# Optimization experiments

Hardware: AMD Instinct MI355X
Metric: run time of the kernel (lower is better)

## Reference

```python
import jax, jax.numpy as jnp
import numpy as np

B, N = 8, 2048
D_MODEL, D_QK, NHEAD, N_K, D_FF = 256, 128, 8, 16, 1024
LN_EPS = 1e-5


def _layer_norm(x, g, b):
    m = jnp.mean(x, axis=-1, keepdims=True)
    v = jnp.var(x, axis=-1, keepdims=True)
    return (x - m) * jax.lax.rsqrt(v + LN_EPS) * g + b


def _l2_normalize(x):
    # F.normalize(dim=-1): x / max(||x||_2, 1e-12)
    n = jnp.sqrt(jnp.sum(x * x, axis=-1, keepdims=True))
    return x / jnp.maximum(n, 1e-12)


def setup_inputs() -> dict:
    key = jax.random.key(0)
    ks = jax.random.split(key, 12)
    s = 0.02
    return {
        "x": jax.random.normal(ks[0], (B, N, D_MODEL), dtype=jnp.float32),
        # linear_q / linear_k (d_model -> d_model_qk)
        "Wq": jax.random.normal(ks[1], (D_MODEL, D_QK), dtype=jnp.float32) * s,
        "bq": jnp.zeros((D_QK,), jnp.float32),
        "Wk": jax.random.normal(ks[2], (D_MODEL, D_QK), dtype=jnp.float32) * s,
        "bk": jnp.zeros((D_QK,), jnp.float32),
        # NoLinearQKMHA: value + output projections (d_model -> d_model)
        "Wv": jax.random.normal(ks[3], (D_MODEL, D_MODEL), dtype=jnp.float32) * s,
        "bv": jnp.zeros((D_MODEL,), jnp.float32),
        "Wo": jax.random.normal(ks[4], (D_MODEL, D_MODEL), dtype=jnp.float32) * s,
        "bo": jnp.zeros((D_MODEL,), jnp.float32),
        # norm1 (applied to gathered values)
        "g1": jnp.ones((D_MODEL,), jnp.float32),
        "b1": jnp.zeros((D_MODEL,), jnp.float32),
        # ffn: LayerNorm -> Linear -> GELU -> Linear
        "gf": jnp.ones((D_MODEL,), jnp.float32),
        "bf": jnp.zeros((D_MODEL,), jnp.float32),
        "W1": jax.random.normal(ks[5], (D_MODEL, D_FF), dtype=jnp.float32) * s,
        "b1f": jnp.zeros((D_FF,), jnp.float32),
        "W2": jax.random.normal(ks[6], (D_FF, D_MODEL), dtype=jnp.float32) * s,
        "b2f": jnp.zeros((D_MODEL,), jnp.float32),
        # residual_weight (init 0 in torch; nonzero here for a meaningful baseline)
        "rw": jnp.full((1,), 0.5, jnp.float32),
    }


def reference(x, Wq, bq, Wk, bk, Wv, bv, Wo, bo, g1, b1, gf, bf, W1, b1f, W2, b2f, rw):
    # --- project + normalize queries/keys ---
    qn = _l2_normalize(x @ Wq + bq)   # [B,N,Dqk]
    kn = _l2_normalize(x @ Wk + bk)   # [B,N,Dqk]

    # --- KNN: k smallest Euclidean distances from each query to keys ---
    d2 = (jnp.sum(qn * qn, -1)[:, :, None]
          + jnp.sum(kn * kn, -1)[:, None, :]
          - 2.0 * jnp.einsum('bqd,bkd->bqk', qn, kn))   # [B,N,N]
    _, idx = jax.lax.top_k(-d2, N_K)                     # [B,N,n_k]

    # --- gather neighbors ---
    gather = jax.vmap(lambda arr, ind: arr[ind])
    x_v = gather(x, idx)    # [B,N,n_k,D_MODEL]
    x_k = gather(kn, idx)   # [B,N,n_k,Dqk]

    # --- windowed MHA (NoLinearQK: q,k used directly; v projected) ---
    xnorm = _layer_norm(x_v, g1, b1)
    v = xnorm @ Wv + bv                                  # [B,N,n_k,D_MODEL]
    dh, dv = D_QK // NHEAD, D_MODEL // NHEAD
    qh = qn.reshape(B, N, NHEAD, dh)
    kh = x_k.reshape(B, N, N_K, NHEAD, dh)
    vh = v.reshape(B, N, N_K, NHEAD, dv)
    logits = jnp.einsum('bnhd,bnkhd->bnhk', qh, kh) / np.float32(np.sqrt(dh))
    attn = jax.nn.softmax(logits, axis=-1)
    o = jnp.einsum('bnhk,bnkhe->bnhe', attn, vh).reshape(B, N, D_MODEL)
    o = o @ Wo + bo

    # --- residuals (eval: dropout = identity) ---
    x = x + o * rw
    h = _layer_norm(x, gf, bf) @ W1 + b1f
    h = jax.nn.gelu(h, approximate=False) @ W2 + b2f
    x = x + h * rw
    return x
```

## Files before the change

kernel.cpp:

```cpp
#include <hip/hip_runtime.h>
#include <math.h>

#define BATCH 8
#define SEQ   2048
#define DM    256
#define DQK   128
#define NHEADS 8
#define NK    16
#define DFF   1024

typedef __attribute__((ext_vector_type(8))) short short8;
typedef __attribute__((ext_vector_type(8))) _Float16 half8;
typedef __attribute__((ext_vector_type(4))) float floatx4;
typedef unsigned long long ull;

__device__ __forceinline__ unsigned short f2bf(float f) {
    unsigned int u = __float_as_uint(f);
    u += 0x7fffu + ((u >> 16) & 1u);
    return (unsigned short)(u >> 16);
}

__device__ __forceinline__ float gelu_fast(float h) {
    float y = 0.7978845608028654f * (h + 0.044715f * h * h * h);
    float e = __expf(2.f * y);
    float t = 1.f - 2.f / (e + 1.f);
    return 0.5f * h * (1.f + t);
}

__device__ __forceinline__ ull mkkey(float f, int gidx) {
    unsigned int u = __float_as_uint(f);
    u ^= (unsigned int)((int)u >> 31) | 0x80000000u;
    return ((ull)u << 32) | (unsigned int)(2047 - gidx);
}

__device__ __forceinline__ ull shfl_xor_u64(ull v, int m) {
    unsigned int lo = (unsigned int)v, hi = (unsigned int)(v >> 32);
    lo = __shfl_xor(lo, m);
    hi = __shfl_xor(hi, m);
    return ((ull)hi << 32) | lo;
}

__global__ __launch_bounds__(256) void conv_kernel(
    const float* __restrict__ W1, const float* __restrict__ W2,
    const float* __restrict__ Wv, const float* __restrict__ Wo,
    unsigned short* __restrict__ W1f, unsigned short* __restrict__ W2f,
    unsigned short* __restrict__ Wvf, unsigned short* __restrict__ Wof)
{
    int g = blockIdx.x * 256 + threadIdx.x;
    const float* W; unsigned short* O; int e, stride;
    if (g < 32768)      { W = W1; O = W1f; e = g;         stride = DFF; }
    else if (g < 65536) { W = W2; O = W2f; e = g - 32768; stride = DM;  }
    else if (g < 73728) { W = Wv; O = Wvf; e = g - 65536; stride = DM;  }
    else                { W = Wo; O = Wof; e = g - 73728; stride = DM;  }
    int lane = e & 63;
    int kk, nt;
    if (g < 32768)      { kk = (e >> 6) & 7;  nt = e >> 9;  }
    else if (g < 65536) { kk = (e >> 6) & 31; nt = e >> 11; }
    else                { kk = (e >> 6) & 7;  nt = e >> 9;  }
    int n = nt * 16 + (lane & 15);
    int k0 = kk * 32 + (lane >> 4) * 8;
    unsigned int pk[4];
    #pragma unroll
    for (int jj = 0; jj < 4; ++jj) {
        unsigned short lo = f2bf(W[(size_t)(k0 + 2 * jj) * stride + n]);
        unsigned short hi = f2bf(W[(size_t)(k0 + 2 * jj + 1) * stride + n]);
        pk[jj] = (unsigned int)lo | ((unsigned int)hi << 16);
    }
    *(uint4*)(O + (size_t)e * 8) = make_uint4(pk[0], pk[1], pk[2], pk[3]);
}

__global__ __launch_bounds__(256) void proj_qk_kernel(
    const float* __restrict__ x,
    const float* __restrict__ Wq, const float* __restrict__ bq,
    const float* __restrict__ Wk, const float* __restrict__ bk,
    float* __restrict__ qn, float* __restrict__ kn,
    unsigned short* __restrict__ knTh, unsigned short* __restrict__ knTl,
    float* __restrict__ knsq)
{
    __shared__ __align__(16) float xs[8 * 256];
    __shared__ __align__(16) float ks[8 * 128];
    __shared__ float nred[8][2], kred[8][2], k2red[8][2];

    const int tid = threadIdx.x;
    const int b = blockIdx.x & 7;
    const int chunk = blockIdx.x >> 3;
    const size_t t0 = (size_t)b * SEQ + (size_t)chunk * 8;

    for (int i = tid; i < 8 * 256; i += 256) xs[i] = x[t0 * DM + i];
    __syncthreads();

    {
        const int col = tid & 127, half = tid >> 7;
        float qa[4] = {0.f, 0.f, 0.f, 0.f}, ka[4] = {0.f, 0.f, 0.f, 0.f};
        for (int d = 0; d < 256; ++d) {
            float wq = Wq[d * DQK + col];
            float wk = Wk[d * DQK + col];
            #pragma unroll
            for (int t = 0; t < 4; ++t) {
                float xv = xs[(half * 4 + t) * 256 + d];
                qa[t] = fmaf(xv, wq, qa[t]);
                ka[t] = fmaf(xv, wk, ka[t]);
            }
        }
        #pragma unroll
        for (int t = 0; t < 4; ++t) { qa[t] += bq[col]; ka[t] += bk[col]; }

        const int sub = (tid >> 6) & 1;
        #pragma unroll
        for (int t = 0; t < 4; ++t) {
            float sq = qa[t] * qa[t], sk = ka[t] * ka[t];
            #pragma unroll
            for (int m = 1; m < 64; m <<= 1) { sq += __shfl_xor(sq, m); sk += __shfl_xor(sk, m); }
            if ((tid & 63) == 0) { nred[half * 4 + t][sub] = sq; kred[half * 4 + t][sub] = sk; }
        }
        __syncthreads();
        float kvv[4];
        #pragma unroll
        for (int t = 0; t < 4; ++t) {
            int tok = half * 4 + t;
            float nq = sqrtf(nred[tok][0] + nred[tok][1]);
            float nk = sqrtf(kred[tok][0] + kred[tok][1]);
            float qv = qa[t] / fmaxf(nq, 1e-12f);
            float kv = ka[t] / fmaxf(nk, 1e-12f);
            qn[(t0 + tok) * DQK + col] = qv;
            kn[(t0 + tok) * DQK + col] = kv;
            ks[tok * 128 + col] = kv;
            kvv[t] = kv;
        }
        #pragma unroll
        for (int t = 0; t < 4; ++t) {
            float s2 = kvv[t] * kvv[t];
            #pragma unroll
            for (int m = 1; m < 64; m <<= 1) s2 += __shfl_xor(s2, m);
            if ((tid & 63) == 0) k2red[half * 4 + t][sub] = s2;
        }
        __syncthreads();
        if (tid < 8) knsq[t0 + tid] = k2red[tid][0] + k2red[tid][1];
    }

    {
        const int e   = tid & 127;
        const int sel = tid >> 7;
        const int key = e & 7;
        const int kq  = e >> 3;
        const int kk  = kq >> 2, qd = kq & 3;
        const int nt  = chunk >> 1;
        const int n   = ((chunk & 1) << 3) + key;
        const float* src = &ks[key * 128 + kk * 32 + qd * 8];
        unsigned int pk[4];
        #pragma unroll
        for (int jj = 0; jj < 4; ++jj) {
            float v0 = src[2 * jj], v1 = src[2 * jj + 1];
            _Float16 h0 = (_Float16)v0, h1 = (_Float16)v1;
            unsigned short u0, u1;
            if (sel == 0) {
                u0 = __builtin_bit_cast(unsigned short, h0);
                u1 = __builtin_bit_cast(unsigned short, h1);
            } else {
                _Float16 l0 = (_Float16)((v0 - (float)h0) * 4096.f);
                _Float16 l1 = (_Float16)((v1 - (float)h1) * 4096.f);
                u0 = __builtin_bit_cast(unsigned short, l0);
                u1 = __builtin_bit_cast(unsigned short, l1);
            }
            pk[jj] = (unsigned int)u0 | ((unsigned int)u1 << 16);
        }
        unsigned short* dst = (sel ? knTl : knTh)
            + (size_t)b * 262144
            + (size_t)((nt * 4 + kk) * 64 + qd * 16 + n) * 8;
        *(uint4*)dst = make_uint4(pk[0], pk[1], pk[2], pk[3]);
    }
}

__global__ __launch_bounds__(256) void proj_v_kernel(
    const float* __restrict__ x,
    const float* __restrict__ bv, const float* __restrict__ g1,
    const float* __restrict__ b1,
    const unsigned short* __restrict__ Wvf, float* __restrict__ vall)
{
    __shared__ __align__(16) float xs[16][260];
    __shared__ float stat_m[16], stat_r[16];
    __shared__ float bvs[256], g1s[256], b1s[256];

    const int tid = threadIdx.x;
    const int lane = tid & 63, wave = tid >> 6;
    const int quad = lane >> 4, lr = lane & 15;
    const size_t t0 = (size_t)blockIdx.x * 16;

    for (int i = tid; i < 16 * 256; i += 256) xs[i >> 8][i & 255] = x[t0 * DM + i];
    bvs[tid] = bv[tid]; g1s[tid] = g1[tid]; b1s[tid] = b1[tid];
    __syncthreads();

    {
        int tok = tid >> 4, l = tid & 15;
        float s = 0.f, s2 = 0.f;
        #pragma unroll
        for (int i = 0; i < 16; ++i) {
            float v = xs[tok][l + 16 * i];
            s += v; s2 += v * v;
        }
        #pragma unroll
        for (int m = 1; m < 16; m <<= 1) { s += __shfl_xor(s, m); s2 += __shfl_xor(s2, m); }
        if (l == 0) {
            float mean = s * (1.f / 256.f);
            float var  = s2 * (1.f / 256.f) - mean * mean;
            stat_m[tok] = mean;
            stat_r[tok] = rsqrtf(var + 1e-5f);
        }
    }
    __syncthreads();

    short8 av[8];
    {
        float mm = stat_m[lr], rr = stat_r[lr];
        #pragma unroll
        for (int kk = 0; kk < 8; ++kk) {
            #pragma unroll
            for (int j = 0; j < 8; ++j) {
                int k = kk * 32 + quad * 8 + j;
                float v = (xs[lr][k] - mm) * rr * g1s[k] + b1s[k];
                av[kk][j] = (short)f2bf(v);
            }
        }
    }
    floatx4 acc[4];
    #pragma unroll
    for (int nt = 0; nt < 4; ++nt) acc[nt] = (floatx4){0.f, 0.f, 0.f, 0.f};
    #pragma unroll
    for (int nt = 0; nt < 4; ++nt) {
        #pragma unroll
        for (int kk = 0; kk < 8; ++kk) {
            short8 bfr = *(const short8*)(Wvf + ((size_t)(((wave * 4 + nt) * 8 + kk) * 64) + lane) * 8);
            acc[nt] = __builtin_amdgcn_mfma_f32_16x16x32_bf16(av[kk], bfr, acc[nt], 0, 0, 0);
        }
    }
    #pragma unroll
    for (int nt = 0; nt < 4; ++nt) {
        int col = (wave * 4 + nt) * 16 + lr;
        float bb = bvs[col];
        #pragma unroll
        for (int reg = 0; reg < 4; ++reg) {
            int row = quad * 4 + reg;
            vall[(t0 + row) * DM + col] = acc[nt][reg] + bb;
        }
    }
}

__global__ __launch_bounds__(256, 4) void attn_kernel(
    const float* __restrict__ x,
    const float* __restrict__ qn_g, const float* __restrict__ kn_g,
    const unsigned short* __restrict__ knTh, const unsigned short* __restrict__ knTl,
    const float* __restrict__ knsq_g,
    const float* __restrict__ vall,
    const unsigned short* __restrict__ Wof, const float* __restrict__ bo,
    const float* __restrict__ rw, float* __restrict__ out)
{
    __shared__ __align__(16) float s_ld[16 * 512];
    float* attn_s = s_ld;
    float* o8     = s_ld + 2048;

    const int tid = threadIdx.x;
    const int lane = tid & 63, wave = tid >> 6;
    const int quad = lane >> 4, lr = lane & 15;
    const int sg = lane >> 5, sl = lane & 31;
    const int sgid = wave * 2 + sg;
    const int b = blockIdx.x & 7;
    const int chunk = blockIdx.x >> 3;
    const size_t tq0 = (size_t)b * SEQ + (size_t)chunk * 16;
    const size_t rowb = (size_t)b * SEQ;

    half8 a_hi[4], a_lo[4];
    {
        const float* qrow = qn_g + (tq0 + lr) * DQK + quad * 8;
        #pragma unroll
        for (int kk = 0; kk < 4; ++kk) {
            float4 fa = *(const float4*)(qrow + kk * 32);
            float4 fb = *(const float4*)(qrow + kk * 32 + 4);
            float vv[8] = {fa.x, fa.y, fa.z, fa.w, fb.x, fb.y, fb.z, fb.w};
            #pragma unroll
            for (int j = 0; j < 8; ++j) {
                float v = vv[j];
                _Float16 h = (_Float16)v;
                a_hi[kk][j] = h;
                a_lo[kk][j] = (_Float16)((v - (float)h) * 4096.f);
            }
        }
    }

    const unsigned short* bh = knTh + (size_t)b * 262144;
    const unsigned short* bl = knTl + (size_t)b * 262144;
    const float* ksqb = knsq_g + rowb;

    ull c0[2], c1[2];

    for (int q4 = 0; q4 < 4; ++q4) {
        if (q4) __syncthreads();

        for (int t = 0; t < 8; ++t) {
            const int tile = q4 * 32 + wave * 8 + t;
            const unsigned short* ph = bh + (size_t)tile * 2048 + lane * 8;
            const unsigned short* pl = bl + (size_t)tile * 2048 + lane * 8;
            floatx4 am  = (floatx4){0.f, 0.f, 0.f, 0.f};
            floatx4 ax1 = (floatx4){0.f, 0.f, 0.f, 0.f};
            floatx4 ax2 = (floatx4){0.f, 0.f, 0.f, 0.f};
            #pragma unroll
            for (int kk = 0; kk < 4; ++kk) {
                half8 bhf = *(const half8*)(ph + kk * 512);
                half8 blf = *(const half8*)(pl + kk * 512);
                am  = __builtin_amdgcn_mfma_f32_16x16x32_f16(a_hi[kk], bhf, am,  0, 0, 0);
                ax1 = __builtin_amdgcn_mfma_f32_16x16x32_f16(a_hi[kk], blf, ax1, 0, 0, 0);
                ax2 = __builtin_amdgcn_mfma_f32_16x16x32_f16(a_lo[kk], bhf, ax2, 0, 0, 0);
            }
            const int keyloc = (wave * 8 + t) * 16 + lr;
            const float kq = ksqb[q4 * 512 + keyloc];
            #pragma unroll
            for (int r = 0; r < 4; ++r) {
                s_ld[(quad * 4 + r) * 512 + keyloc] =
                    2.f * (am[r] + (ax1[r] + ax2[r]) * (1.f / 4096.f)) - kq;
            }
        }
        __syncthreads();

        #pragma unroll
        for (int qi = 0; qi < 2; ++qi) {
            const int q = sgid + 8 * qi;
            const float* srow = &s_ld[q * 512 + sl];
            float f0 = -INFINITY, f1 = -INFINITY;
            int   i0 = 0, i1 = 0;
            #pragma unroll
            for (int i = 0; i < 16; ++i) {
                float f = srow[32 * i];
                int gidx = q4 * 512 + sl + 32 * i;
                bool a  = f > f0;
                bool bb = f > f1;
                f1 = a ? f0 : (bb ? f    : f1);
                i1 = a ? i0 : (bb ? gidx : i1);
                f0 = a ? f    : f0;
                i0 = a ? gidx : i0;
            }
            ull k2v = mkkey(f1, i1);
            ull cur = mkkey(f0, i0);
            int cnt = 0;
            for (int r = 0; r < NK; ++r) {
                ull w = cur;
                #pragma unroll
                for (int m = 1; m < 32; m <<= 1) {
                    ull o = shfl_xor_u64(w, m);
                    if (o > w) w = o;
                }
                const int slot = q4 * 16 + r;
                if (sl == slot)      c0[qi] = w;
                if (sl == slot - 32) c1[qi] = w;
                if (cur == w) {
                    ++cnt;
                    if (cnt == 1) cur = k2v;
                    else {
                        ull best = 0;
                        #pragma unroll
                        for (int i = 0; i < 16; ++i) {
                            float f = srow[32 * i];
                            ull k = mkkey(f, q4 * 512 + sl + 32 * i);
                            if (k < w && k > best) best = k;
                        }
                        cur = best;
                    }
                }
            }
        }
    }
    __syncthreads();

    int tidx[2] = {0, 0};
    #pragma unroll
    for (int qi = 0; qi < 2; ++qi) {
        ull ca = c0[qi], cb = c1[qi];
        ull hi = ca > cb ? ca : cb;
        ull lo = ca > cb ? cb : ca;
        ull cur = hi;
        int cnt = 0;
        for (int r = 0; r < NK; ++r) {
            ull w = cur;
            #pragma unroll
            for (int m = 1; m < 32; m <<= 1) {
                ull o = shfl_xor_u64(w, m);
                if (o > w) w = o;
            }
            if (sl == r) tidx[qi] = 2047 - (int)(unsigned int)(w & 0xFFFFFFFFull);
            if (cur == w) { ++cnt; cur = (cnt == 1) ? lo : 0ull; }
        }
    }

    #pragma unroll
    for (int qq = 0; qq < 4; ++qq) {
        const int sgq = qq & 1;
        const int qiq = qq >> 1;
        const int q   = wave * 2 + sgq + 8 * qiq;
        const int srcb = sgq * 32;
        const int h = lane >> 3;
        const int k1 = lane & 7, k2 = 8 + (lane & 7);
        const int i1 = __shfl(tidx[qiq], srcb + k1);
        const int i2 = __shfl(tidx[qiq], srcb + k2);
        const float* qrow = qn_g + (tq0 + q) * DQK + h * 16;
        const float* kr1 = kn_g + (rowb + i1) * DQK + h * 16;
        const float* kr2 = kn_g + (rowb + i2) * DQK + h * 16;
        float lg1 = 0.f, lg2 = 0.f;
        #pragma unroll
        for (int d = 0; d < 16; d += 4) {
            float4 qv = *(const float4*)&qrow[d];
            float4 a1 = *(const float4*)&kr1[d];
            float4 a2 = *(const float4*)&kr2[d];
            lg1 = fmaf(qv.x, a1.x, lg1); lg1 = fmaf(qv.y, a1.y, lg1);
            lg1 = fmaf(qv.z, a1.z, lg1); lg1 = fmaf(qv.w, a1.w, lg1);
            lg2 = fmaf(qv.x, a2.x, lg2); lg2 = fmaf(qv.y, a2.y, lg2);
            lg2 = fmaf(qv.z, a2.z, lg2); lg2 = fmaf(qv.w, a2.w, lg2);
        }
        lg1 *= 0.25f; lg2 *= 0.25f;
        float mx = fmaxf(lg1, lg2);
        #pragma unroll
        for (int m = 1; m < 8; m <<= 1) mx = fmaxf(mx, __shfl_xor(mx, m));
        float e1 = expf(lg1 - mx), e2 = expf(lg2 - mx);
        float ssum = e1 + e2;
        #pragma unroll
        for (int m = 1; m < 8; m <<= 1) ssum += __shfl_xor(ssum, m);
        attn_s[q * 128 + h * 16 + k1] = e1 / ssum;
        attn_s[q * 128 + h * 16 + k2] = e2 / ssum;

        float o[4] = {0.f, 0.f, 0.f, 0.f};
        for (int k = 0; k < NK; ++k) {
            const int ik = __shfl(tidx[qiq], srcb + k);
            const float* vr = vall + (rowb + ik) * DM;
            #pragma unroll
            for (int j = 0; j < 4; ++j) {
                int d = lane + 64 * j;
                o[j] = fmaf(attn_s[q * 128 + (d >> 5) * 16 + k], vr[d], o[j]);
            }
        }
        #pragma unroll
        for (int j = 0; j < 4; ++j) o8[q * 260 + lane + 64 * j] = o[j];
    }
    __syncthreads();

    {
        short8 ao[8];
        #pragma unroll
        for (int kk = 0; kk < 8; ++kk) {
            #pragma unroll
            for (int j = 0; j < 8; ++j) {
                int k = kk * 32 + quad * 8 + j;
                ao[kk][j] = (short)f2bf(o8[lr * 260 + k]);
            }
        }
        floatx4 aw[4];
        #pragma unroll
        for (int nt = 0; nt < 4; ++nt) aw[nt] = (floatx4){0.f, 0.f, 0.f, 0.f};
        #pragma unroll
        for (int nt = 0; nt < 4; ++nt) {
            #pragma unroll
            for (int kk = 0; kk < 8; ++kk) {
                short8 bofr = *(const short8*)(Wof + ((size_t)(((wave * 4 + nt) * 8 + kk) * 64) + lane) * 8);
                aw[nt] = __builtin_amdgcn_mfma_f32_16x16x32_bf16(ao[kk], bofr, aw[nt], 0, 0, 0);
            }
        }
        float rwv = rw[0];
        #pragma unroll
        for (int nt = 0; nt < 4; ++nt) {
            int col = (wave * 4 + nt) * 16 + lr;
            float bov = bo[col];
            #pragma unroll
            for (int reg = 0; reg < 4; ++reg) {
                int row = quad * 4 + reg;
                size_t t = tq0 + row;
                out[t * DM + col] = x[t * DM + col] + (aw[nt][reg] + bov) * rwv;
            }
        }
    }
}

__global__ __launch_bounds__(512, 1) void ffn_kernel(
    float* __restrict__ io,
    const float* __restrict__ gf, const float* __restrict__ bf,
    const unsigned short* __restrict__ W1f, const float* __restrict__ b1f,
    const unsigned short* __restrict__ W2f, const float* __restrict__ b2f,
    const float* __restrict__ rw)
{
    __shared__ __align__(16) float xs[32][260];
    __shared__ float gfs[256], bfs[256], b2s[256], b1s[1024];
    __shared__ float stat_m[32], stat_r[32];
    __shared__ __align__(16) unsigned short Af[2][8 * 64 * 8];
    __shared__ __align__(16) unsigned short G[32][1032];

    const int tid = threadIdx.x;
    const int lane = tid & 63, wave = tid >> 6;
    const int quad = lane >> 4, lr = lane & 15;
    const size_t t0 = (size_t)blockIdx.x * 32;

    for (int i = tid; i < 32 * 256; i += 512) xs[i >> 8][i & 255] = io[t0 * DM + i];
    if (tid < 256) { gfs[tid] = gf[tid]; bfs[tid] = bf[tid]; b2s[tid] = b2f[tid]; }
    for (int i = tid; i < 1024; i += 512) b1s[i] = b1f[i];
    __syncthreads();

    {
        int tok = tid >> 4, l = tid & 15;
        float s = 0.f, s2 = 0.f;
        #pragma unroll
        for (int i = 0; i < 16; ++i) {
            float v = xs[tok][l + 16 * i];
            s += v; s2 += v * v;
        }
        #pragma unroll
        for (int m = 1; m < 16; m <<= 1) { s += __shfl_xor(s, m); s2 += __shfl_xor(s2, m); }
        if (l == 0) {
            float mean = s * (1.f / 256.f);
            float var  = s2 * (1.f / 256.f) - mean * mean;
            stat_m[tok] = mean;
            stat_r[tok] = rsqrtf(var + 1e-5f);
        }
    }
    __syncthreads();

    {
        const int rt = wave >> 2;
        for (int kk = wave & 3; kk < 8; kk += 4) {
            int m = rt * 16 + lr, k0 = kk * 32 + quad * 8;
            float mm = stat_m[m], rr = stat_r[m];
            unsigned int pk[4];
            #pragma unroll
            for (int jj = 0; jj < 4; ++jj) {
                int ka = k0 + 2 * jj, kb = ka + 1;
                float v0 = (xs[m][ka] - mm) * rr * gfs[ka] + bfs[ka];
                float v1 = (xs[m][kb] - mm) * rr * gfs[kb] + bfs[kb];
                pk[jj] = (unsigned int)f2bf(v0) | ((unsigned int)f2bf(v1) << 16);
            }
            *(uint4*)&Af[rt][(kk * 64 + lane) * 8] = make_uint4(pk[0], pk[1], pk[2], pk[3]);
        }
    }
    __syncthreads();

    short8 afr[2][8];
    #pragma unroll
    for (int rt = 0; rt < 2; ++rt)
        #pragma unroll
        for (int kk = 0; kk < 8; ++kk)
            afr[rt][kk] = *(const short8*)&Af[rt][(kk * 64 + lane) * 8];

    for (int nt = 0; nt < 8; ++nt) {
        floatx4 acc0 = (floatx4){0.f, 0.f, 0.f, 0.f};
        floatx4 acc1 = (floatx4){0.f, 0.f, 0.f, 0.f};
        const int ntg = wave * 8 + nt;
        #pragma unroll
        for (int kk = 0; kk < 8; ++kk) {
            short8 bfr = *(const short8*)(W1f + (size_t)((ntg * 8 + kk) * 64 + lane) * 8);
            acc0 = __builtin_amdgcn_mfma_f32_16x16x32_bf16(afr[0][kk], bfr, acc0, 0, 0, 0);
            acc1 = __builtin_amdgcn_mfma_f32_16x16x32_bf16(afr[1][kk], bfr, acc1, 0, 0, 0);
        }
        const int n = ntg * 16 + lr;
        const float bb = b1s[n];
        #pragma unroll
        for (int reg = 0; reg < 4; ++reg) {
            int row = quad * 4 + reg;
            G[row][n]      = f2bf(gelu_fast(acc0[reg] + bb));
            G[row + 16][n] = f2bf(gelu_fast(acc1[reg] + bb));
        }
    }
    __syncthreads();

    floatx4 acc2[2][2];
    #pragma unroll
    for (int nt2 = 0; nt2 < 2; ++nt2)
        #pragma unroll
        for (int rt = 0; rt < 2; ++rt)
            acc2[nt2][rt] = (floatx4){0.f, 0.f, 0.f, 0.f};

    for (int kk2 = 0; kk2 < 32; ++kk2) {
        short8 a20 = *(const short8*)&G[lr][kk2 * 32 + quad * 8];
        short8 a21 = *(const short8*)&G[16 + lr][kk2 * 32 + quad * 8];
        #pragma unroll
        for (int nt2 = 0; nt2 < 2; ++nt2) {
            short8 b2 = *(const short8*)(W2f + (size_t)((((wave * 2 + nt2) * 32 + kk2) * 64 + lane) * 8));
            acc2[nt2][0] = __builtin_amdgcn_mfma_f32_16x16x32_bf16(a20, b2, acc2[nt2][0], 0, 0, 0);
            acc2[nt2][1] = __builtin_amdgcn_mfma_f32_16x16x32_bf16(a21, b2, acc2[nt2][1], 0, 0, 0);
        }
    }

    float rwv = rw[0];
    #pragma unroll
    for (int nt2 = 0; nt2 < 2; ++nt2) {
        int col = (wave * 2 + nt2) * 16 + lr;
        float bb = b2s[col];
        #pragma unroll
        for (int rt = 0; rt < 2; ++rt) {
            #pragma unroll
            for (int reg = 0; reg < 4; ++reg) {
                int row = rt * 16 + quad * 4 + reg;
                float o = acc2[nt2][rt][reg] + bb;
                io[(t0 + row) * DM + col] = xs[row][col] + o * rwv;
            }
        }
    }
}

extern "C" void kernel_launch(void* const* d_in, const int* in_sizes, int n_in,
                              void* d_out, int out_size, void* d_ws, size_t ws_size,
                              hipStream_t stream)
{
    const float* x   = (const float*)d_in[0];
    const float* Wq  = (const float*)d_in[1];
    const float* bq  = (const float*)d_in[2];
    const float* Wk  = (const float*)d_in[3];
    const float* bk  = (const float*)d_in[4];
    const float* Wv  = (const float*)d_in[5];
    const float* bv  = (const float*)d_in[6];
    const float* Wo  = (const float*)d_in[7];
    const float* bo  = (const float*)d_in[8];
    const float* g1  = (const float*)d_in[9];
    const float* b1  = (const float*)d_in[10];
    const float* gf  = (const float*)d_in[11];
    const float* bf  = (const float*)d_in[12];
    const float* W1  = (const float*)d_in[13];
    const float* b1f = (const float*)d_in[14];
    const float* W2  = (const float*)d_in[15];
    const float* b2f = (const float*)d_in[16];
    const float* rw  = (const float*)d_in[17];
    float* out = (float*)d_out;

    float* ws   = (float*)d_ws;
    float* qn   = ws;
    float* kn   = ws + 2097152;
    unsigned short* knTh = (unsigned short*)(ws + 4194304);
    unsigned short* knTl = knTh + 2097152;
    float* vall = ws + 6291456;
    float* knsq = ws + 10485760;
    unsigned short* W1f = (unsigned short*)(ws + 10502144);
    unsigned short* W2f = W1f + 262144;
    unsigned short* Wvf = W2f + 262144;
    unsigned short* Wof = Wvf + 65536;

    conv_kernel<<<320, 256, 0, stream>>>(W1, W2, Wv, Wo, W1f, W2f, Wvf, Wof);
    proj_qk_kernel<<<BATCH * SEQ / 8, 256, 0, stream>>>(x, Wq, bq, Wk, bk,
                                                        qn, kn, knTh, knTl, knsq);
    proj_v_kernel<<<BATCH * SEQ / 16, 256, 0, stream>>>(x, bv, g1, b1, Wvf, vall);
    attn_kernel<<<BATCH * SEQ / 16, 256, 0, stream>>>(x, qn, kn, knTh, knTl, knsq, vall,
                                                      Wof, bo, rw, out);
    ffn_kernel<<<BATCH * SEQ / 32, 512, 0, stream>>>(out, gf, bf, W1f, b1f, W2f, b2f, rw);
}
```

Measured before the change: 346.3 us.

## Alias FFN shared buffers to raise occupancy; read x directly in QK projection

The FFN kernel now places xs, Af and G in one aliased shared-memory pool and raises the launch bound to 4 blocks per CU. This shrinks LDS use so more blocks can be resident at once. Because G overwrites xs, the residual add now reloads x from global memory, and an extra barrier protects the aliasing. The QK projection kernel drops its shared staging of x and instead has each thread load float4 rows straight from global memory, removing one barrier and the LDS round trip at the cost of more global reads.

```diff
diff --git a/kernel.cpp b/kernel.cpp
--- a/kernel.cpp
+++ b/kernel.cpp
@@ -77,7 +77,6 @@
     unsigned short* __restrict__ knTh, unsigned short* __restrict__ knTl,
     float* __restrict__ knsq)
 {
-    __shared__ __align__(16) float xs[8 * 256];
     __shared__ __align__(16) float ks[8 * 128];
     __shared__ float nred[8][2], kred[8][2], k2red[8][2];
 
@@ -86,20 +85,30 @@
     const int chunk = blockIdx.x >> 3;
     const size_t t0 = (size_t)b * SEQ + (size_t)chunk * 8;
 
-    for (int i = tid; i < 8 * 256; i += 256) xs[i] = x[t0 * DM + i];
-    __syncthreads();
-
     {
         const int col = tid & 127, half = tid >> 7;
+        const int half_u = __builtin_amdgcn_readfirstlane(half);
+        const float* xrow[4];
+        #pragma unroll
+        for (int t = 0; t < 4; ++t)
+            xrow[t] = x + (t0 + (size_t)(half_u * 4 + t)) * DM;
+
         float qa[4] = {0.f, 0.f, 0.f, 0.f}, ka[4] = {0.f, 0.f, 0.f, 0.f};
-        for (int d = 0; d < 256; ++d) {
-            float wq = Wq[d * DQK + col];
-            float wk = Wk[d * DQK + col];
-            #pragma unroll
-            for (int t = 0; t < 4; ++t) {
-                float xv = xs[(half * 4 + t) * 256 + d];
-                qa[t] = fmaf(xv, wq, qa[t]);
-                ka[t] = fmaf(xv, wk, ka[t]);
+        for (int d = 0; d < 256; d += 4) {
+            float4 xv[4];
+            #pragma unroll
+            for (int t = 0; t < 4; ++t) xv[t] = *(const float4*)(xrow[t] + d);
+            #pragma unroll
+            for (int dd = 0; dd < 4; ++dd) {
+                float wq = Wq[(d + dd) * DQK + col];
+                float wk = Wk[(d + dd) * DQK + col];
+                #pragma unroll
+                for (int t = 0; t < 4; ++t) {
+                    float xval = (dd == 0) ? xv[t].x : (dd == 1) ? xv[t].y
+                               : (dd == 2) ? xv[t].z : xv[t].w;
+                    qa[t] = fmaf(xval, wq, qa[t]);
+                    ka[t] = fmaf(xval, wk, ka[t]);
+                }
             }
         }
         #pragma unroll
@@ -475,18 +484,20 @@
     }
 }
 
-__global__ __launch_bounds__(512, 1) void ffn_kernel(
+__global__ __launch_bounds__(512, 4) void ffn_kernel(
     float* __restrict__ io,
     const float* __restrict__ gf, const float* __restrict__ bf,
     const unsigned short* __restrict__ W1f, const float* __restrict__ b1f,
     const unsigned short* __restrict__ W2f, const float* __restrict__ b2f,
     const float* __restrict__ rw)
 {
-    __shared__ __align__(16) float xs[32][260];
+    __shared__ __align__(16) char pool[66048];
     __shared__ float gfs[256], bfs[256], b2s[256], b1s[1024];
     __shared__ float stat_m[32], stat_r[32];
-    __shared__ __align__(16) unsigned short Af[2][8 * 64 * 8];
-    __shared__ __align__(16) unsigned short G[32][1032];
+
+    float (*xs)[260] = (float(*)[260])pool;
+    unsigned short (*Af)[8 * 64 * 8] = (unsigned short(*)[8 * 64 * 8])(pool + 33280);
+    unsigned short (*G)[1032] = (unsigned short(*)[1032])pool;
 
     const int tid = threadIdx.x;
     const int lane = tid & 63, wave = tid >> 6;
@@ -541,6 +552,7 @@
         #pragma unroll
         for (int kk = 0; kk < 8; ++kk)
             afr[rt][kk] = *(const short8*)&Af[rt][(kk * 64 + lane) * 8];
+    __syncthreads();
 
     for (int nt = 0; nt < 8; ++nt) {
         floatx4 acc0 = (floatx4){0.f, 0.f, 0.f, 0.f};
@@ -592,7 +604,8 @@
             for (int reg = 0; reg < 4; ++reg) {
                 int row = rt * 16 + quad * 4 + reg;
                 float o = acc2[nt2][rt][reg] + bb;
-                io[(t0 + row) * DM + col] = xs[row][col] + o * rwv;
+                size_t idx = (t0 + row) * DM + col;
+                io[idx] = io[idx] + o * rwv;
             }
         }
     }
```

After: 339.2 us (median of 2 runs). -2.1%, faster.
